# Kernel tuning notes

Hardware: AMD Instinct MI355X
Metric: run time of the kernel (lower is better)

The kernel has to match this reference:

```python
import jax, jax.numpy as jnp
import numpy as np

B, S, D, H = 4, 2048, 1024, 16
HD = D // H  # head dim = 64


def setup_inputs() -> dict:
    key = jax.random.key(0)
    ks = jax.random.split(key, 9)
    scale = 1.0 / np.sqrt(D)
    return {
        "x": jax.random.normal(ks[0], (B, S, D), dtype=jnp.float32),
        "Wq": jax.random.normal(ks[1], (D, D), dtype=jnp.float32) * scale,
        "bq": jnp.zeros((D,), dtype=jnp.float32),
        "Wk": jax.random.normal(ks[2], (D, D), dtype=jnp.float32) * scale,
        "bk": jnp.zeros((D,), dtype=jnp.float32),
        "Wv": jax.random.normal(ks[3], (D, D), dtype=jnp.float32) * scale,
        "bv": jnp.zeros((D,), dtype=jnp.float32),
        "Wo": jax.random.normal(ks[4], (D, D), dtype=jnp.float32) * scale,
        "bo": jnp.zeros((D,), dtype=jnp.float32),
    }


def _split_heads(t):
    # [B,S,D] -> [B,H,S,HD]
    return t.reshape(t.shape[0], t.shape[1], H, HD).transpose(0, 2, 1, 3)


def reference(x, Wq, bq, Wk, bk, Wv, bv, Wo, bo):
    q = _split_heads(x @ Wq + bq)
    k = _split_heads(x @ Wk + bk)
    v = _split_heads(x @ Wv + bv)
    # scaled dot-product attention; scale by sqrt of key dim (= head dim)
    scores = jnp.einsum("bhqd,bhkd->bhqk", q, k) / jnp.sqrt(jnp.asarray(HD, q.dtype))
    weights = jax.nn.softmax(scores, axis=-1)
    attn = jnp.einsum("bhqk,bhkd->bhqd", weights, v)
    concat = attn.transpose(0, 2, 1, 3).reshape(x.shape[0], -1, D)
    out = concat @ Wo + bo
    return out, weights
```

## Files before the change

### kernel.cpp

```cpp
#include <hip/hip_runtime.h>
#include <cstddef>
#include <cstdint>

static constexpr int BB = 4;
static constexpr int SS = 2048;
static constexpr int DD = 1024;
static constexpr int HH = 16;
static constexpr int HDIM = 64;
static constexpr int MROWS = BB * SS;

typedef __attribute__((ext_vector_type(4))) float f32x4;
typedef __bf16 bf16x8 __attribute__((ext_vector_type(8)));
typedef __bf16 bf16x4 __attribute__((ext_vector_type(4)));

#define GLB_U32(p) ((const __attribute__((address_space(1))) uint32_t*)(p))
#define LDS_U32(p) ((__attribute__((address_space(3))) uint32_t*)(p))

__device__ __forceinline__ float fexp2(float x) {
#if __has_builtin(__builtin_amdgcn_exp2f)
    return __builtin_amdgcn_exp2f(x);
#else
    return exp2f(x);
#endif
}

__global__ __launch_bounds__(256) void cvt_x(const float* __restrict__ x,
                                             __bf16* __restrict__ xb)
{
    size_t i = ((size_t)blockIdx.x * 256 + threadIdx.x) * 8;
    float4 a = *reinterpret_cast<const float4*>(x + i);
    float4 b = *reinterpret_cast<const float4*>(x + i + 4);
    bf16x8 v;
    v[0] = (__bf16)a.x; v[1] = (__bf16)a.y; v[2] = (__bf16)a.z; v[3] = (__bf16)a.w;
    v[4] = (__bf16)b.x; v[5] = (__bf16)b.y; v[6] = (__bf16)b.z; v[7] = (__bf16)b.w;
    *reinterpret_cast<bf16x8*>(xb + i) = v;
}

__global__ __launch_bounds__(256) void transpose_w(
    const float* __restrict__ W0, const float* __restrict__ W1,
    const float* __restrict__ W2, const float* __restrict__ W3,
    __bf16* __restrict__ wt_base)
{
    const float* W = (blockIdx.z == 0) ? W0 : (blockIdx.z == 1) ? W1
                   : (blockIdx.z == 2) ? W2 : W3;
    __bf16* WT = wt_base + (size_t)blockIdx.z * 1048576;

    __shared__ float T[64][68];
    const int t = threadIdx.x;
    const int n0 = blockIdx.x * 64, k0 = blockIdx.y * 64;

#pragma unroll
    for (int it = 0; it < 4; ++it) {
        const int row = it * 16 + (t >> 4);
        const int col = (t & 15) * 4;
        float4 v = *reinterpret_cast<const float4*>(&W[(size_t)(k0 + row) * 1024 + n0 + col]);
        T[row][col + 0] = v.x; T[row][col + 1] = v.y;
        T[row][col + 2] = v.z; T[row][col + 3] = v.w;
    }
    __syncthreads();

#pragma unroll
    for (int it = 0; it < 2; ++it) {
        const int idx = it * 256 + t;
        const int n = idx >> 3, ch = idx & 7;
        bf16x8 v;
#pragma unroll
        for (int e = 0; e < 8; ++e) v[e] = (__bf16)T[ch * 8 + e][n];
        *reinterpret_cast<bf16x8*>(&WT[(size_t)(n0 + n) * 1024 + k0 + ch * 8]) = v;
    }
}

template <int MODE>
__global__ __launch_bounds__(256) void gemm_bf16(
    const __bf16* __restrict__ A,
    const __bf16* __restrict__ BT,
    const float* __restrict__ bias,
    void* __restrict__ Cout)
{
    __shared__ __bf16 At[128 * 32];
    __shared__ __bf16 Bt[128 * 32];

    constexpr float OSC = (MODE == 0) ? 0.18033688011112042f : 1.0f;

    const int t = threadIdx.x;
    const int w = t >> 6, l = t & 63, l16 = l & 15, lg = l >> 4;
    const int m0 = blockIdx.x * 128, n0 = blockIdx.y * 128;
    const int wr = w >> 1, wc = w & 1;

    f32x4 acc[4][4] = {};

    for (int k0 = 0; k0 < 1024; k0 += 32) {
#pragma unroll
        for (int r = 0; r < 2; ++r) {
            const int cb = (w * 2 + r) * 64;
            const int ch = cb + l;
            const __bf16* srcA = A + (size_t)(m0 + (ch >> 2)) * 1024 + k0 + (ch & 3) * 8;
            __builtin_amdgcn_global_load_lds(GLB_U32(srcA), LDS_U32(At + cb * 8), 16, 0, 0);
        }
#pragma unroll
        for (int r = 0; r < 2; ++r) {
            const int cb = (w * 2 + r) * 64;
            const int ch = cb + l;
            const __bf16* srcB = BT + (size_t)(n0 + (ch >> 2)) * 1024 + k0 + (ch & 3) * 8;
            __builtin_amdgcn_global_load_lds(GLB_U32(srcB), LDS_U32(Bt + cb * 8), 16, 0, 0);
        }
        __syncthreads();

        bf16x8 af[4], bf[4];
#pragma unroll
        for (int i = 0; i < 4; ++i) {
            af[i] = *reinterpret_cast<const bf16x8*>(At + (wr * 64 + i * 16 + l16) * 32 + lg * 8);
            bf[i] = *reinterpret_cast<const bf16x8*>(Bt + (wc * 64 + i * 16 + l16) * 32 + lg * 8);
        }
#pragma unroll
        for (int i = 0; i < 4; ++i)
#pragma unroll
            for (int j = 0; j < 4; ++j)
                acc[i][j] = __builtin_amdgcn_mfma_f32_16x16x32_bf16(af[i], bf[j], acc[i][j], 0, 0, 0);
        __syncthreads();
    }

    if constexpr (MODE == 2) {
        __shared__ __bf16 Tr[4][64][72];
#pragma unroll
        for (int i = 0; i < 4; ++i)
#pragma unroll
            for (int j = 0; j < 4; ++j)
#pragma unroll
                for (int r = 0; r < 4; ++r) {
                    const int n = n0 + wc * 64 + j * 16 + l16;
                    Tr[w][j * 16 + l16][i * 16 + lg * 4 + r] =
                        (__bf16)(acc[i][j][r] + bias[n]);
                }
        asm volatile("s_waitcnt lgkmcnt(0)" ::: "memory");
        __bf16* V = (__bf16*)Cout;
#pragma unroll
        for (int it = 0; it < 8; ++it) {
            const int idx = it * 64 + l;
            const int np = idx >> 3, c = idx & 7;
            bf16x8 v = *reinterpret_cast<const bf16x8*>(&Tr[w][np][c * 8]);
            const int gn = n0 + wc * 64 + np;
            const int m  = m0 + wr * 64 + c * 8;
            const size_t o = (((size_t)(m >> 11) * HH + (gn >> 6)) * HDIM + (gn & 63)) * SS + (m & 2047);
            *reinterpret_cast<bf16x8*>(V + o) = v;
        }
    } else {
#pragma unroll
        for (int i = 0; i < 4; ++i)
#pragma unroll
            for (int j = 0; j < 4; ++j) {
                const int n = n0 + wc * 64 + j * 16 + l16;
                const float bv = bias[n];
#pragma unroll
                for (int r = 0; r < 4; ++r) {
                    const int m = m0 + wr * 64 + i * 16 + lg * 4 + r;
                    const float v = (acc[i][j][r] + bv) * OSC;
                    if constexpr (MODE == 3) {
                        ((float*)Cout)[(size_t)m * 1024 + n] = v;
                    } else {
                        const size_t o = (((size_t)(m >> 11) * HH + (n >> 6)) * SS + (m & 2047)) * HDIM + (n & 63);
                        ((__bf16*)Cout)[o] = (__bf16)v;
                    }
                }
            }
    }
}

__device__ __forceinline__ void stage64x64(const __bf16* __restrict__ g, int rstride,
                                           __bf16* lds, int t)
{
#pragma unroll
    for (int it = 0; it < 2; ++it) {
        const int i = it * 256 + t;
        const int r = i >> 3, j = i & 7;
        const __bf16* src = g + (size_t)r * rstride + ((j ^ (r & 7)) << 3);
        __builtin_amdgcn_global_load_lds(GLB_U32(src), LDS_U32(lds + i * 8), 16, 0, 0);
    }
}

__device__ __forceinline__ bf16x8 ldsF(const __bf16* buf, int row, int c0)
{
    return *(const bf16x8*)(buf + row * 64 + (((c0 >> 3) ^ (row & 7)) << 3));
}

__global__ __launch_bounds__(256, 4) void attn_fused(
    const __bf16* __restrict__ Qg, const __bf16* __restrict__ Kg,
    const __bf16* __restrict__ VTg, float* __restrict__ Wout,
    __bf16* __restrict__ attnb)
{
    __shared__ __bf16 Ksh[2][64 * 64];
    __shared__ __bf16 Vsh[2][64 * 64];
    __shared__ __bf16 Psh[4][16 * 64];

    const int t = threadIdx.x, w = t >> 6, l = t & 63, l16 = l & 15, lg = l >> 4;

    int bid = (int)blockIdx.x;
    bid = (bid & 7) * 256 + (bid >> 3);
    const int qt = bid & 31, bh = bid >> 5;
    const int qr = qt * 64 + w * 16;

    const __bf16* Qp = Qg + ((size_t)bh * SS + qr) * HDIM;
    const __bf16* Kp = Kg + (size_t)bh * SS * HDIM;
    const __bf16* Vp = VTg + (size_t)bh * HDIM * SS;

    const bf16x8 aq0 = *(const bf16x8*)(Qp + l16 * 64 + lg * 8);
    const bf16x8 aq1 = *(const bf16x8*)(Qp + l16 * 64 + 32 + lg * 8);

    char* pbase = (char*)&Psh[w][0];

    float ssum = 0.f;

    stage64x64(Kp, 64, Ksh[0], t);
    __syncthreads();

    for (int kt = 0; kt < 32; ++kt) {
        if (kt < 31) stage64x64(Kp + (kt + 1) * 4096, 64, Ksh[(kt + 1) & 1], t);
        const __bf16* kb = Ksh[kt & 1];

#pragma unroll
        for (int c4 = 0; c4 < 4; ++c4) {
            const bf16x8 b0 = ldsF(kb, c4 * 16 + l16, lg * 8);
            const bf16x8 b1 = ldsF(kb, c4 * 16 + l16, 32 + lg * 8);
            f32x4 a = {0.f, 0.f, 0.f, 0.f};
            a = __builtin_amdgcn_mfma_f32_16x16x32_bf16(b0, aq0, a, 0, 0, 0);
            a = __builtin_amdgcn_mfma_f32_16x16x32_bf16(b1, aq1, a, 0, 0, 0);
            ssum += (fexp2(a[0]) + fexp2(a[1])) + (fexp2(a[2]) + fexp2(a[3]));
        }
        __syncthreads();
    }

    stage64x64(Kp, 64, Ksh[0], t);
    stage64x64(Vp, SS, Vsh[0], t);

    ssum += __shfl_xor(ssum, 16);
    ssum += __shfl_xor(ssum, 32);
    const float linv = 1.0f / ssum;

    __syncthreads();

    f32x4 o[4] = {};
    float* wbase = Wout + ((size_t)bh * SS + qr + l16) * SS;

    for (int kt = 0; kt < 32; ++kt) {
        if (kt < 31) {
            stage64x64(Kp + (kt + 1) * 4096, 64, Ksh[(kt + 1) & 1], t);
            stage64x64(Vp + (kt + 1) * 64, SS, Vsh[(kt + 1) & 1], t);
        }
        const __bf16* kb = Ksh[kt & 1];
        const __bf16* vb = Vsh[kt & 1];

#pragma unroll
        for (int c4 = 0; c4 < 4; ++c4) {
            const bf16x8 b0 = ldsF(kb, c4 * 16 + l16, lg * 8);
            const bf16x8 b1 = ldsF(kb, c4 * 16 + l16, 32 + lg * 8);
            f32x4 a = {0.f, 0.f, 0.f, 0.f};
            a = __builtin_amdgcn_mfma_f32_16x16x32_bf16(b0, aq0, a, 0, 0, 0);
            a = __builtin_amdgcn_mfma_f32_16x16x32_bf16(b1, aq1, a, 0, 0, 0);
            f32x4 pv;
            pv[0] = fexp2(a[0]) * linv; pv[1] = fexp2(a[1]) * linv;
            pv[2] = fexp2(a[2]) * linv; pv[3] = fexp2(a[3]) * linv;
            __builtin_nontemporal_store(pv,
                (f32x4*)(wbase + kt * 64 + c4 * 16 + lg * 4));
            bf16x4 pk;
            pk[0] = (__bf16)pv[0]; pk[1] = (__bf16)pv[1];
            pk[2] = (__bf16)pv[2]; pk[3] = (__bf16)pv[3];
            const int off = l16 * 128 + ((c4 * 32 + lg * 8) ^ ((l16 & 7) << 4));
            *(bf16x4*)(pbase + off) = pk;
        }
        asm volatile("s_waitcnt lgkmcnt(0)" ::: "memory");
        __builtin_amdgcn_sched_barrier(0);

        bf16x8 pa[2];
#pragma unroll
        for (int kc = 0; kc < 2; ++kc) {
            const int off = l16 * 128 + ((kc * 64 + lg * 16) ^ ((l16 & 7) << 4));
            pa[kc] = *(const bf16x8*)(pbase + off);
        }
#pragma unroll
        for (int nt = 0; nt < 4; ++nt) {
            const bf16x8 bv0 = ldsF(vb, nt * 16 + l16, lg * 8);
            const bf16x8 bv1 = ldsF(vb, nt * 16 + l16, 32 + lg * 8);
            o[nt] = __builtin_amdgcn_mfma_f32_16x16x32_bf16(pa[0], bv0, o[nt], 0, 0, 0);
            o[nt] = __builtin_amdgcn_mfma_f32_16x16x32_bf16(pa[1], bv1, o[nt], 0, 0, 0);
        }
        __syncthreads();
    }

    const int b = bh >> 4, h = bh & 15;
#pragma unroll
    for (int nt = 0; nt < 4; ++nt)
#pragma unroll
        for (int r = 0; r < 4; ++r) {
            const int srow = qr + lg * 4 + r;
            attnb[((size_t)b * SS + srow) * DD + h * 64 + nt * 16 + l16] =
                (__bf16)o[nt][r];
        }
}

extern "C" void kernel_launch(void* const* d_in, const int* in_sizes, int n_in,
                              void* d_out, int out_size, void* d_ws, size_t ws_size,
                              hipStream_t stream)
{
    const float* x  = (const float*)d_in[0];
    const float* Wq = (const float*)d_in[1];
    const float* bq = (const float*)d_in[2];
    const float* Wk = (const float*)d_in[3];
    const float* bk = (const float*)d_in[4];
    const float* Wv = (const float*)d_in[5];
    const float* bv = (const float*)d_in[6];
    const float* Wo = (const float*)d_in[7];
    const float* bo = (const float*)d_in[8];

    float* out     = (float*)d_out;
    float* weights = out + (size_t)BB * SS * DD;

    __bf16* ws = (__bf16*)d_ws;
    const size_t NX = (size_t)MROWS * DD;
    __bf16* xb    = ws;
    __bf16* wtb   = xb + NX;
    __bf16* wqT   = wtb;
    __bf16* wkT   = wtb + 1048576;
    __bf16* wvT   = wtb + 2097152;
    __bf16* woT   = wtb + 3145728;
    __bf16* qb    = wtb + 4194304;
    __bf16* kb    = qb + NX;
    __bf16* vtb   = kb + NX;
    __bf16* attnb = vtb + NX;

    dim3 blk(256);

    cvt_x<<<dim3(4096), blk, 0, stream>>>(x, xb);
    transpose_w<<<dim3(16, 16, 4), blk, 0, stream>>>(Wq, Wk, Wv, Wo, wtb);

    dim3 ggrid(MROWS / 128, DD / 128);
    gemm_bf16<0><<<ggrid, blk, 0, stream>>>(xb, wqT, bq, qb);
    gemm_bf16<1><<<ggrid, blk, 0, stream>>>(xb, wkT, bk, kb);
    gemm_bf16<2><<<ggrid, blk, 0, stream>>>(xb, wvT, bv, vtb);

    attn_fused<<<dim3(2048), blk, 0, stream>>>(qb, kb, vtb, weights, attnb);

    gemm_bf16<3><<<ggrid, blk, 0, stream>>>(attnb, woT, bo, out);
}
```

Baseline: 435.1 us.

## Fuse QKV GEMMs, vectorize epilogues, triple-buffer K pass with finer waits

```diff
diff --git a/kernel.cpp b/kernel.cpp
--- a/kernel.cpp
+++ b/kernel.cpp
@@ -70,17 +70,115 @@
     }
 }
 
-template <int MODE>
-__global__ __launch_bounds__(256) void gemm_bf16(
-    const __bf16* __restrict__ A,
-    const __bf16* __restrict__ BT,
-    const float* __restrict__ bias,
-    void* __restrict__ Cout)
-{
-    __shared__ __bf16 At[128 * 32];
-    __shared__ __bf16 Bt[128 * 32];
-
-    constexpr float OSC = (MODE == 0) ? 0.18033688011112042f : 1.0f;
+__global__ __launch_bounds__(256) void gemm_qkv(
+    const __bf16* __restrict__ xb, const __bf16* __restrict__ wt,
+    const float* __restrict__ bq, const float* __restrict__ bk,
+    const float* __restrict__ bv,
+    __bf16* __restrict__ qb, __bf16* __restrict__ kb, __bf16* __restrict__ vtb)
+{
+    __shared__ __bf16 AB[2 * 128 * 32];
+    __bf16* At = AB;
+    __bf16* Bt = AB + 4096;
+
+    const int t = threadIdx.x;
+    const int w = t >> 6, l = t & 63, l16 = l & 15, lg = l >> 4;
+    const int m0 = blockIdx.x * 128;
+    const int sel = blockIdx.y >> 3;
+    const int n0 = (blockIdx.y & 7) * 128;
+    const int wr = w >> 1, wc = w & 1;
+
+    const __bf16* BT = wt + (size_t)sel * 1048576;
+    const float* bias = (sel == 0) ? bq : (sel == 1) ? bk : bv;
+
+    f32x4 acc[4][4] = {};
+
+    for (int k0 = 0; k0 < 1024; k0 += 32) {
+#pragma unroll
+        for (int r = 0; r < 2; ++r) {
+            const int cb = (w * 2 + r) * 64;
+            const int ch = cb + l;
+            const __bf16* srcA = xb + (size_t)(m0 + (ch >> 2)) * 1024 + k0 + (ch & 3) * 8;
+            __builtin_amdgcn_global_load_lds(GLB_U32(srcA), LDS_U32(At + cb * 8), 16, 0, 0);
+        }
+#pragma unroll
+        for (int r = 0; r < 2; ++r) {
+            const int cb = (w * 2 + r) * 64;
+            const int ch = cb + l;
+            const __bf16* srcB = BT + (size_t)(n0 + (ch >> 2)) * 1024 + k0 + (ch & 3) * 8;
+            __builtin_amdgcn_global_load_lds(GLB_U32(srcB), LDS_U32(Bt + cb * 8), 16, 0, 0);
+        }
+        __syncthreads();
+
+        bf16x8 af[4], bf[4];
+#pragma unroll
+        for (int i = 0; i < 4; ++i) {
+            af[i] = *reinterpret_cast<const bf16x8*>(At + (wr * 64 + i * 16 + l16) * 32 + lg * 8);
+            bf[i] = *reinterpret_cast<const bf16x8*>(Bt + (wc * 64 + i * 16 + l16) * 32 + lg * 8);
+        }
+#pragma unroll
+        for (int i = 0; i < 4; ++i)
+#pragma unroll
+            for (int j = 0; j < 4; ++j)
+                acc[i][j] = __builtin_amdgcn_mfma_f32_16x16x32_bf16(af[i], bf[j], acc[i][j], 0, 0, 0);
+        __syncthreads();
+    }
+
+    const float osc = (sel == 0) ? 0.18033688011112042f : 1.0f;
+
+    if (sel < 2) {
+        __bf16* Et = AB + w * 2048;
+        __bf16* outp = (sel == 0) ? qb : kb;
+#pragma unroll
+        for (int j = 0; j < 4; ++j) {
+            const float bvv = bias[n0 + wc * 64 + j * 16 + l16];
+#pragma unroll
+            for (int i = 0; i < 4; ++i)
+#pragma unroll
+                for (int r = 0; r < 4; ++r)
+                    Et[(i * 16 + lg * 4 + r) * 24 + l16] =
+                        (__bf16)((acc[i][j][r] + bvv) * osc);
+#pragma unroll
+            for (int it = 0; it < 2; ++it) {
+                const int idx = it * 64 + l;
+                const int ml = idx >> 1, ch = idx & 1;
+                bf16x8 v = *(const bf16x8*)(Et + ml * 24 + ch * 8);
+                const int M = m0 + wr * 64 + ml;
+                const int N = n0 + wc * 64 + j * 16 + ch * 8;
+                *(bf16x8*)(outp + (((size_t)(M >> 11) * HH + (N >> 6)) * SS
+                                   + (M & 2047)) * HDIM + (N & 63)) = v;
+            }
+        }
+    } else {
+        __bf16* Et = AB + w * 2048;
+#pragma unroll
+        for (int j = 0; j < 4; ++j) {
+            const float bvv = bias[n0 + wc * 64 + j * 16 + l16];
+#pragma unroll
+            for (int i = 0; i < 4; ++i)
+#pragma unroll
+                for (int r = 0; r < 4; ++r)
+                    Et[l16 * 72 + i * 16 + lg * 4 + r] = (__bf16)(acc[i][j][r] + bvv);
+#pragma unroll
+            for (int it = 0; it < 2; ++it) {
+                const int idx = it * 64 + l;
+                const int row = idx >> 3, ch = idx & 7;
+                bf16x8 v = *(const bf16x8*)(Et + row * 72 + ch * 8);
+                const int N = n0 + wc * 64 + j * 16 + row;
+                const int M = m0 + wr * 64 + ch * 8;
+                *(bf16x8*)(vtb + (((size_t)(M >> 11) * HH + (N >> 6)) * HDIM
+                                  + (N & 63)) * SS + (M & 2047)) = v;
+            }
+        }
+    }
+}
+
+__global__ __launch_bounds__(256) void gemm_out(
+    const __bf16* __restrict__ A, const __bf16* __restrict__ BT,
+    const float* __restrict__ bias, float* __restrict__ C)
+{
+    __shared__ __bf16 AB[2 * 128 * 32];
+    __bf16* At = AB;
+    __bf16* Bt = AB + 4096;
 
     const int t = threadIdx.x;
     const int w = t >> 6, l = t & 63, l16 = l & 15, lg = l >> 4;
@@ -120,49 +218,24 @@
         __syncthreads();
     }
 
-    if constexpr (MODE == 2) {
-        __shared__ __bf16 Tr[4][64][72];
+    float* Et = (float*)AB + w * 1024;
+#pragma unroll
+    for (int j = 0; j < 4; ++j) {
+        const float bvv = bias[n0 + wc * 64 + j * 16 + l16];
 #pragma unroll
         for (int i = 0; i < 4; ++i)
 #pragma unroll
-            for (int j = 0; j < 4; ++j)
-#pragma unroll
-                for (int r = 0; r < 4; ++r) {
-                    const int n = n0 + wc * 64 + j * 16 + l16;
-                    Tr[w][j * 16 + l16][i * 16 + lg * 4 + r] =
-                        (__bf16)(acc[i][j][r] + bias[n]);
-                }
-        asm volatile("s_waitcnt lgkmcnt(0)" ::: "memory");
-        __bf16* V = (__bf16*)Cout;
-#pragma unroll
-        for (int it = 0; it < 8; ++it) {
+            for (int r = 0; r < 4; ++r)
+                Et[(i * 16 + lg * 4 + r) * 16 + l16] = acc[i][j][r] + bvv;
+#pragma unroll
+        for (int it = 0; it < 4; ++it) {
             const int idx = it * 64 + l;
-            const int np = idx >> 3, c = idx & 7;
-            bf16x8 v = *reinterpret_cast<const bf16x8*>(&Tr[w][np][c * 8]);
-            const int gn = n0 + wc * 64 + np;
-            const int m  = m0 + wr * 64 + c * 8;
-            const size_t o = (((size_t)(m >> 11) * HH + (gn >> 6)) * HDIM + (gn & 63)) * SS + (m & 2047);
-            *reinterpret_cast<bf16x8*>(V + o) = v;
-        }
-    } else {
-#pragma unroll
-        for (int i = 0; i < 4; ++i)
-#pragma unroll
-            for (int j = 0; j < 4; ++j) {
-                const int n = n0 + wc * 64 + j * 16 + l16;
-                const float bv = bias[n];
-#pragma unroll
-                for (int r = 0; r < 4; ++r) {
-                    const int m = m0 + wr * 64 + i * 16 + lg * 4 + r;
-                    const float v = (acc[i][j][r] + bv) * OSC;
-                    if constexpr (MODE == 3) {
-                        ((float*)Cout)[(size_t)m * 1024 + n] = v;
-                    } else {
-                        const size_t o = (((size_t)(m >> 11) * HH + (n >> 6)) * SS + (m & 2047)) * HDIM + (n & 63);
-                        ((__bf16*)Cout)[o] = (__bf16)v;
-                    }
-                }
-            }
+            const int ml = idx >> 2, ch = idx & 3;
+            float4 v = *(const float4*)(Et + ml * 16 + ch * 4);
+            const int M = m0 + wr * 64 + ml;
+            const int N = n0 + wc * 64 + j * 16 + ch * 4;
+            *(float4*)(C + (size_t)M * 1024 + N) = v;
+        }
     }
 }
 
@@ -188,9 +261,9 @@
     const __bf16* __restrict__ VTg, float* __restrict__ Wout,
     __bf16* __restrict__ attnb)
 {
-    __shared__ __bf16 Ksh[2][64 * 64];
+    __shared__ __bf16 Ksh[3][64 * 64];
     __shared__ __bf16 Vsh[2][64 * 64];
-    __shared__ __bf16 Psh[4][16 * 64];
+    __shared__ __bf16 Psh[4][1280];
 
     const int t = threadIdx.x, w = t >> 6, l = t & 63, l16 = l & 15, lg = l >> 4;
 
@@ -211,12 +284,16 @@
     float ssum = 0.f;
 
     stage64x64(Kp, 64, Ksh[0], t);
+    stage64x64(Kp + 4096, 64, Ksh[1], t);
     __syncthreads();
 
     for (int kt = 0; kt < 32; ++kt) {
-        if (kt < 31) stage64x64(Kp + (kt + 1) * 4096, 64, Ksh[(kt + 1) & 1], t);
-        const __bf16* kb = Ksh[kt & 1];
-
+        if (kt < 30)
+            stage64x64(Kp + (kt + 2) * 4096, 64, Ksh[(kt + 2) % 3], t);
+        __builtin_amdgcn_sched_barrier(0);
+        const __bf16* kb = Ksh[kt % 3];
+
+        __builtin_amdgcn_s_setprio(1);
 #pragma unroll
         for (int c4 = 0; c4 < 4; ++c4) {
             const bf16x8 b0 = ldsF(kb, c4 * 16 + l16, lg * 8);
@@ -226,7 +303,12 @@
             a = __builtin_amdgcn_mfma_f32_16x16x32_bf16(b1, aq1, a, 0, 0, 0);
             ssum += (fexp2(a[0]) + fexp2(a[1])) + (fexp2(a[2]) + fexp2(a[3]));
         }
-        __syncthreads();
+        __builtin_amdgcn_s_setprio(0);
+
+        if (kt < 30) { asm volatile("s_waitcnt vmcnt(2)" ::: "memory"); }
+        else         { asm volatile("s_waitcnt vmcnt(0)" ::: "memory"); }
+        __builtin_amdgcn_s_barrier();
+        __builtin_amdgcn_sched_barrier(0);
     }
 
     stage64x64(Kp, 64, Ksh[0], t);
@@ -246,9 +328,11 @@
             stage64x64(Kp + (kt + 1) * 4096, 64, Ksh[(kt + 1) & 1], t);
             stage64x64(Vp + (kt + 1) * 64, SS, Vsh[(kt + 1) & 1], t);
         }
+        __builtin_amdgcn_sched_barrier(0);
         const __bf16* kb = Ksh[kt & 1];
         const __bf16* vb = Vsh[kt & 1];
 
+        __builtin_amdgcn_s_setprio(1);
 #pragma unroll
         for (int c4 = 0; c4 < 4; ++c4) {
             const bf16x8 b0 = ldsF(kb, c4 * 16 + l16, lg * 8);
@@ -267,6 +351,7 @@
             const int off = l16 * 128 + ((c4 * 32 + lg * 8) ^ ((l16 & 7) << 4));
             *(bf16x4*)(pbase + off) = pk;
         }
+        __builtin_amdgcn_s_setprio(0);
         asm volatile("s_waitcnt lgkmcnt(0)" ::: "memory");
         __builtin_amdgcn_sched_barrier(0);
 
@@ -276,6 +361,7 @@
             const int off = l16 * 128 + ((kc * 64 + lg * 16) ^ ((l16 & 7) << 4));
             pa[kc] = *(const bf16x8*)(pbase + off);
         }
+        __builtin_amdgcn_s_setprio(1);
 #pragma unroll
         for (int nt = 0; nt < 4; ++nt) {
             const bf16x8 bv0 = ldsF(vb, nt * 16 + l16, lg * 8);
@@ -283,18 +369,27 @@
             o[nt] = __builtin_amdgcn_mfma_f32_16x16x32_bf16(pa[0], bv0, o[nt], 0, 0, 0);
             o[nt] = __builtin_amdgcn_mfma_f32_16x16x32_bf16(pa[1], bv1, o[nt], 0, 0, 0);
         }
-        __syncthreads();
+        __builtin_amdgcn_s_setprio(0);
+
+        asm volatile("s_waitcnt vmcnt(4)" ::: "memory");
+        __builtin_amdgcn_s_barrier();
+        __builtin_amdgcn_sched_barrier(0);
     }
 
     const int b = bh >> 4, h = bh & 15;
+    __bf16* Pe = &Psh[w][0];
 #pragma unroll
     for (int nt = 0; nt < 4; ++nt)
 #pragma unroll
-        for (int r = 0; r < 4; ++r) {
-            const int srow = qr + lg * 4 + r;
-            attnb[((size_t)b * SS + srow) * DD + h * 64 + nt * 16 + l16] =
-                (__bf16)o[nt][r];
-        }
+        for (int r = 0; r < 4; ++r)
+            Pe[(lg * 4 + r) * 80 + nt * 16 + l16] = (__bf16)o[nt][r];
+#pragma unroll
+    for (int it = 0; it < 2; ++it) {
+        const int idx = it * 64 + l;
+        const int row = idx >> 3, ch = idx & 7;
+        bf16x8 v = *(const bf16x8*)(Pe + row * 80 + ch * 8);
+        *(bf16x8*)(attnb + ((size_t)b * SS + qr + row) * DD + h * 64 + ch * 8) = v;
+    }
 }
 
 extern "C" void kernel_launch(void* const* d_in, const int* in_sizes, int n_in,
@@ -318,9 +413,6 @@
     const size_t NX = (size_t)MROWS * DD;
     __bf16* xb    = ws;
     __bf16* wtb   = xb + NX;
-    __bf16* wqT   = wtb;
-    __bf16* wkT   = wtb + 1048576;
-    __bf16* wvT   = wtb + 2097152;
     __bf16* woT   = wtb + 3145728;
     __bf16* qb    = wtb + 4194304;
     __bf16* kb    = qb + NX;
@@ -332,12 +424,9 @@
     cvt_x<<<dim3(4096), blk, 0, stream>>>(x, xb);
     transpose_w<<<dim3(16, 16, 4), blk, 0, stream>>>(Wq, Wk, Wv, Wo, wtb);
 
-    dim3 ggrid(MROWS / 128, DD / 128);
-    gemm_bf16<0><<<ggrid, blk, 0, stream>>>(xb, wqT, bq, qb);
-    gemm_bf16<1><<<ggrid, blk, 0, stream>>>(xb, wkT, bk, kb);
-    gemm_bf16<2><<<ggrid, blk, 0, stream>>>(xb, wvT, bv, vtb);
+    gemm_qkv<<<dim3(64, 24), blk, 0, stream>>>(xb, wtb, bq, bk, bv, qb, kb, vtb);
 
     attn_fused<<<dim3(2048), blk, 0, stream>>>(qb, kb, vtb, weights, attnb);
 
-    gemm_bf16<3><<<ggrid, blk, 0, stream>>>(attnb, woT, bo, out);
-}
+    gemm_out<<<dim3(64, 8), blk, 0, stream>>>(attnb, woT, bo, out);
+}
```

Measured after the change: 444.6 us. 2.2% more time.
